# Performance work log

Hardware: AMD Instinct MI355X
Metric: run time of the kernel (lower is better)

## Reference

```python
import jax, jax.numpy as jnp
import numpy as np

N_S, N_T, E = 50000, 50000, 600000
D_IN, D_H, D_OUT = 256, 128, 64


def setup_inputs() -> dict:
    key = jax.random.key(0)
    k1, k2, k3, k4, k5, k6 = jax.random.split(key, 6)
    edge_src = jax.random.randint(k1, (E,), 0, N_S, dtype=jnp.int32)
    edge_dst = jax.random.randint(k2, (E,), 0, N_T, dtype=jnp.int32)
    edge_index = jnp.stack([edge_src, edge_dst], axis=0)  # [2, E]
    x_s = jax.random.normal(k3, (N_S, D_IN), dtype=jnp.float32)
    x_t = jax.random.normal(k4, (N_T, D_IN), dtype=jnp.float32)
    W0 = jax.random.normal(k5, (D_IN, D_H), dtype=jnp.float32) * (1.0 / np.sqrt(D_IN))
    W1 = jax.random.normal(k6, (D_H, D_OUT), dtype=jnp.float32) * (1.0 / np.sqrt(D_H))
    return {"edge_index": edge_index, "x_s": x_s, "x_t": x_t, "W0": W0, "W1": W1}


def gcn_conv(x, src, dst, W):
    """PyG GCNConv, bias=False: D^{-1/2}(A+I)D^{-1/2} (x @ W)."""
    N = x.shape[0]
    h = x @ W  # [N, out]
    loops = jnp.arange(N, dtype=src.dtype)
    s = jnp.concatenate([src, loops])  # add self-loops
    d = jnp.concatenate([dst, loops])
    deg = jax.ops.segment_sum(jnp.ones_like(d, dtype=h.dtype), d, num_segments=N)
    dinv = jnp.where(deg > 0, jax.lax.rsqrt(deg), 0.0)
    norm = dinv[s] * dinv[d]  # [E+N]
    return jax.ops.segment_sum(h[s] * norm[:, None], d, num_segments=N)


def reference(edge_index, x_s, x_t, W0, W1):
    n_s = x_s.shape[0]
    src = edge_index[0]
    dst = edge_index[1] + n_s  # targets live in the x_t block
    acts = [jax.nn.relu, lambda v: v]
    Ws = [W0, W1]
    for W, act in zip(Ws, acts):
        x = jnp.concatenate([x_s, x_t], axis=0)
        x = act(gcn_conv(x, src, dst, W))
        x_s, x_t = x[:n_s], x[n_s:]
    return (x_s, x_t)
```

## Files before the change

### kernel.cpp

```cpp
#include <hip/hip_runtime.h>
#include <cstdint>
#include <cstddef>

typedef unsigned short u16;
typedef unsigned int   u32;
typedef __attribute__((ext_vector_type(8))) short bf16x8;
typedef __attribute__((ext_vector_type(4))) float f32x4;

#define D_IN  256
#define D_H   128
#define D_OUT 64
#define LSTR  72

__device__ __forceinline__ float bf2f(u16 u){
  union { u32 i; float f; } v; v.i = ((u32)u) << 16; return v.f;
}
__device__ __forceinline__ u16 f2bf(float f){
  union { float f; u32 i; } v; v.f = f;
  u32 r = (v.i + 0x7fffu + ((v.i >> 16) & 1u)) >> 16;
  return (u16)r;
}

__global__ void k_wprep(const float* __restrict__ W0, const float* __restrict__ W1,
                        u16* __restrict__ W0t, u16* __restrict__ W1t,
                        int* __restrict__ deg, int n_t){
  int i = blockIdx.x * 256 + threadIdx.x;
  if (i < 128 * 256){
    int n = i >> 8, k = i & 255;
    W0t[i] = f2bf(W0[(size_t)k * 128 + n]);
  } else if (i < 128 * 256 + 64 * 128){
    int j = i - 128 * 256;
    int n = j >> 7, k = j & 127;
    W1t[j] = f2bf(W1[(size_t)k * 64 + n]);
  } else if (i - (128 * 256 + 64 * 128) < n_t){
    deg[i - (128 * 256 + 64 * 128)] = 0;
  }
}

__global__ void k_deg(const int* __restrict__ dst, int E, int* __restrict__ deg){
  int e = blockIdx.x * 256 + threadIdx.x;
  if (e < E) atomicAdd(&deg[dst[e]], 1);
}

__global__ __launch_bounds__(256) void k_bsum(const int* __restrict__ deg, int N,
                                              int* __restrict__ bsum){
  __shared__ int s[256];
  int tid = threadIdx.x;
  int i = blockIdx.x * 256 + tid;
  s[tid] = (i < N) ? deg[i] : 0;
  __syncthreads();
  for (int o = 128; o > 0; o >>= 1){
    if (tid < o) s[tid] += s[tid + o];
    __syncthreads();
  }
  if (tid == 0) bsum[blockIdx.x] = s[0];
}

__global__ __launch_bounds__(256) void k_off(const int* __restrict__ deg, int N,
                                             const int* __restrict__ bsum, int nb,
                                             int* __restrict__ off, int* __restrict__ cursor,
                                             float* __restrict__ dinv){
  __shared__ int s[256];
  __shared__ int sbase[256];
  const int tid = threadIdx.x;
  const int bid = blockIdx.x;
  const int i   = bid * 256 + tid;
  int acc = 0;
  for (int j = tid; j < bid; j += 256) acc += bsum[j];
  sbase[tid] = acc;
  int v = (i < N) ? deg[i] : 0;
  s[tid] = v;
  __syncthreads();
  for (int o = 128; o > 0; o >>= 1){
    if (tid < o) sbase[tid] += sbase[tid + o];
    __syncthreads();
  }
  for (int o = 1; o < 256; o <<= 1){
    int t = (tid >= o) ? s[tid - o] : 0;
    __syncthreads();
    s[tid] += t;
    __syncthreads();
  }
  if (i < N){
    int excl = s[tid] - v + sbase[0];
    off[i] = excl;
    cursor[i] = excl;
    dinv[i] = rsqrtf((float)v + 1.0f);
  }
}

__global__ void k_fill(const int* __restrict__ src, const int* __restrict__ dst,
                       int E, int* __restrict__ cursor, int* __restrict__ csr){
  int e = blockIdx.x * 256 + threadIdx.x;
  if (e < E){
    int d = dst[e];
    int p = atomicAdd(&cursor[d], 1);
    csr[p] = src[e];
  }
}

__global__ __launch_bounds__(256) void k_gemm1(
    const float* __restrict__ Xs, const float* __restrict__ Xt,
    const u16* __restrict__ W0t, int M, int n_s,
    u16* __restrict__ out)
{
  __shared__ u16 As[128 * LSTR];
  __shared__ u16 Bs[128 * LSTR];
  const int t    = threadIdx.x;
  const int wave = t >> 6, lane = t & 63;
  const int wm   = (wave >> 1) * 64, wn = (wave & 1) * 64;
  const int lm   = lane & 15, quad = lane >> 4;
  const int row0 = blockIdx.x * 128;

  f32x4 acc[4][4];
  const f32x4 z = {0.f, 0.f, 0.f, 0.f};
  #pragma unroll
  for (int i = 0; i < 4; i++)
    #pragma unroll
    for (int j = 0; j < 4; j++) acc[i][j] = z;

  const int ar = t >> 1;
  const int kh = (t & 1) * 32;
  const int r  = row0 + ar;
  const float* xp = nullptr;
  if (r < M) xp = (r < n_s) ? (Xs + (size_t)r * D_IN) : (Xt + (size_t)(r - n_s) * D_IN);
  const u16* wrow = W0t + (size_t)ar * D_IN + kh;

  float4 a4[8];
  int4   b4[4];
  if (xp){
    #pragma unroll
    for (int j = 0; j < 8; j++) a4[j] = *(const float4*)(xp + kh + j * 4);
  } else {
    float4 zz = make_float4(0,0,0,0);
    #pragma unroll
    for (int j = 0; j < 8; j++) a4[j] = zz;
  }
  #pragma unroll
  for (int j = 0; j < 4; j++) b4[j] = *(const int4*)(wrow + j * 8);

  for (int k0 = 0; k0 < D_IN; k0 += 64){
    __syncthreads();
    {
      u16 abuf[32];
      #pragma unroll
      for (int j = 0; j < 8; j++){
        abuf[j*4+0] = f2bf(a4[j].x); abuf[j*4+1] = f2bf(a4[j].y);
        abuf[j*4+2] = f2bf(a4[j].z); abuf[j*4+3] = f2bf(a4[j].w);
      }
      u16* ap = &As[ar * LSTR + kh];
      *(int4*)(ap +  0) = *(int4*)&abuf[0];
      *(int4*)(ap +  8) = *(int4*)&abuf[8];
      *(int4*)(ap + 16) = *(int4*)&abuf[16];
      *(int4*)(ap + 24) = *(int4*)&abuf[24];
      u16* bp = &Bs[ar * LSTR + kh];
      *(int4*)(bp +  0) = b4[0];
      *(int4*)(bp +  8) = b4[1];
      *(int4*)(bp + 16) = b4[2];
      *(int4*)(bp + 24) = b4[3];
    }
    __syncthreads();

    if (k0 + 64 < D_IN){
      if (xp){
        #pragma unroll
        for (int j = 0; j < 8; j++) a4[j] = *(const float4*)(xp + k0 + 64 + kh + j * 4);
      }
      #pragma unroll
      for (int j = 0; j < 4; j++) b4[j] = *(const int4*)(wrow + k0 + 64 + j * 8);
    }

    #pragma unroll
    for (int kk = 0; kk < 64; kk += 32){
      bf16x8 af[4], bfr[4];
      #pragma unroll
      for (int i = 0; i < 4; i++)
        af[i] = *(const bf16x8*)&As[(wm + i*16 + lm) * LSTR + kk + quad*8];
      #pragma unroll
      for (int i = 0; i < 4; i++)
        bfr[i] = *(const bf16x8*)&Bs[(wn + i*16 + lm) * LSTR + kk + quad*8];
      #pragma unroll
      for (int mi = 0; mi < 4; mi++)
        #pragma unroll
        for (int ni = 0; ni < 4; ni++)
          acc[mi][ni] = __builtin_amdgcn_mfma_f32_16x16x32_bf16(
              af[mi], bfr[ni], acc[mi][ni], 0, 0, 0);
    }
  }

  #pragma unroll
  for (int mi = 0; mi < 4; mi++){
    int rbase = row0 + wm + mi * 16 + quad * 4;
    #pragma unroll
    for (int rr = 0; rr < 4; rr++){
      int m = rbase + rr;
      if (m >= M) continue;
      u16* op = out + (size_t)m * D_H + wn + lm;
      #pragma unroll
      for (int ni = 0; ni < 4; ni++)
        op[ni * 16] = f2bf(acc[mi][ni][rr]);
    }
  }
}

__global__ __launch_bounds__(256) void k_aggf(
    const int* __restrict__ off, const int* __restrict__ deg,
    const int* __restrict__ csr, const float* __restrict__ dinv,
    u16* __restrict__ h1, int n_s, int n_t)
{
  int w    = (blockIdx.x * 256 + threadIdx.x) >> 6;
  int lane = threadIdx.x & 63;
  if (w >= n_t) return;
  const int g = lane >> 4;
  const int c = lane & 15;
  int start = off[w];
  int n     = deg[w];

  float r[8], p[8];
  #pragma unroll
  for (int q = 0; q < 8; q++){ r[q] = 0.f; p[q] = 0.f; }

  int i = 0;
  for (; i + 8 <= n; i += 8){
    int sa = csr[start + i + g];
    int sb = csr[start + i + 4 + g];
    int4 da = *(const int4*)(h1 + (size_t)sa * D_H + c * 8);
    int4 db = *(const int4*)(h1 + (size_t)sb * D_H + c * 8);
    const u16* ha = (const u16*)&da;
    const u16* hb = (const u16*)&db;
    #pragma unroll
    for (int q = 0; q < 8; q++){
      float va = bf2f(ha[q]), vb = bf2f(hb[q]);
      r[q] += va + vb;
      p[q] += fmaxf(va, 0.f) + fmaxf(vb, 0.f);
    }
  }
  for (; i < n; i += 4){
    if (i + g < n){
      int sa = csr[start + i + g];
      int4 da = *(const int4*)(h1 + (size_t)sa * D_H + c * 8);
      const u16* ha = (const u16*)&da;
      #pragma unroll
      for (int q = 0; q < 8; q++){
        float va = bf2f(ha[q]);
        r[q] += va;
        p[q] += fmaxf(va, 0.f);
      }
    }
  }

  #pragma unroll
  for (int q = 0; q < 8; q++){
    r[q] += __shfl_xor(r[q], 16, 64);
    r[q] += __shfl_xor(r[q], 32, 64);
    p[q] += __shfl_xor(p[q], 16, 64);
    p[q] += __shfl_xor(p[q], 32, 64);
  }

  if (g == 0){
    float di  = dinv[w];
    float di2 = di * di;
    u16* selfp = h1 + (size_t)(n_s + w) * D_H + c * 8;
    int4 hs = *(const int4*)selfp;
    const u16* hh = (const u16*)&hs;
    u16 ob[8];
    #pragma unroll
    for (int q = 0; q < 8; q++){
      float zq = fmaxf(di * r[q] + di2 * bf2f(hh[q]), 0.f);
      float uq = di * p[q] + di2 * zq;
      ob[q] = f2bf(uq);
    }
    *(int4*)selfp = *(int4*)ob;
  }
}

__global__ __launch_bounds__(256) void k_gemm2(
    const u16* __restrict__ h1, const u16* __restrict__ W1t,
    int M, int n_s, float* __restrict__ out)
{
  __shared__ u16 As[128 * LSTR];
  __shared__ u16 Bs[64 * LSTR];
  const int t    = threadIdx.x;
  const int wave = t >> 6, lane = t & 63;
  const int wm   = wave * 32;
  const int lm   = lane & 15, quad = lane >> 4;
  const int row0 = blockIdx.x * 128;

  f32x4 acc[2][4];
  const f32x4 z = {0.f, 0.f, 0.f, 0.f};
  #pragma unroll
  for (int i = 0; i < 2; i++)
    #pragma unroll
    for (int j = 0; j < 4; j++) acc[i][j] = z;

  const int ar = t >> 1;
  const int kh = (t & 1) * 32;
  const int r  = row0 + ar;
  const bool relu_a = (r < n_s);
  const int bn = t >> 2;
  const int bk = (t & 3) * 16;

  int4 a4[4], w4[2];
  if (r < M){
    const u16* hp = h1 + (size_t)r * D_H + kh;
    #pragma unroll
    for (int j = 0; j < 4; j++) a4[j] = *(const int4*)(hp + j * 8);
  } else {
    int4 zz = make_int4(0,0,0,0);
    #pragma unroll
    for (int j = 0; j < 4; j++) a4[j] = zz;
  }
  w4[0] = *(const int4*)(W1t + (size_t)bn * D_H + bk);
  w4[1] = *(const int4*)(W1t + (size_t)bn * D_H + bk + 8);

  for (int k0 = 0; k0 < D_H; k0 += 64){
    __syncthreads();
    {
      u16 abuf[32];
      #pragma unroll
      for (int j = 0; j < 4; j++){
        u16* hh = (u16*)&a4[j];
        #pragma unroll
        for (int q = 0; q < 8; q++){
          u16 v = hh[q];
          abuf[j*8+q] = (relu_a && (v & 0x8000u)) ? (u16)0 : v;
        }
      }
      u16* ap = &As[ar * LSTR + kh];
      *(int4*)(ap +  0) = *(int4*)&abuf[0];
      *(int4*)(ap +  8) = *(int4*)&abuf[8];
      *(int4*)(ap + 16) = *(int4*)&abuf[16];
      *(int4*)(ap + 24) = *(int4*)&abuf[24];
      u16* bp = &Bs[bn * LSTR + bk];
      *(int4*)(bp + 0) = w4[0];
      *(int4*)(bp + 8) = w4[1];
    }
    __syncthreads();

    if (k0 + 64 < D_H){
      if (r < M){
        const u16* hp = h1 + (size_t)r * D_H + k0 + 64 + kh;
        #pragma unroll
        for (int j = 0; j < 4; j++) a4[j] = *(const int4*)(hp + j * 8);
      }
      w4[0] = *(const int4*)(W1t + (size_t)bn * D_H + k0 + 64 + bk);
      w4[1] = *(const int4*)(W1t + (size_t)bn * D_H + k0 + 64 + bk + 8);
    }

    #pragma unroll
    for (int kk = 0; kk < 64; kk += 32){
      bf16x8 af[2], bfr[4];
      #pragma unroll
      for (int i = 0; i < 2; i++)
        af[i] = *(const bf16x8*)&As[(wm + i*16 + lm) * LSTR + kk + quad*8];
      #pragma unroll
      for (int i = 0; i < 4; i++)
        bfr[i] = *(const bf16x8*)&Bs[(i*16 + lm) * LSTR + kk + quad*8];
      #pragma unroll
      for (int mi = 0; mi < 2; mi++)
        #pragma unroll
        for (int ni = 0; ni < 4; ni++)
          acc[mi][ni] = __builtin_amdgcn_mfma_f32_16x16x32_bf16(
              af[mi], bfr[ni], acc[mi][ni], 0, 0, 0);
    }
  }

  #pragma unroll
  for (int mi = 0; mi < 2; mi++){
    int rbase = row0 + wm + mi * 16 + quad * 4;
    #pragma unroll
    for (int rr = 0; rr < 4; rr++){
      int m = rbase + rr;
      if (m >= M) continue;
      float* op = out + (size_t)m * D_OUT + lm;
      #pragma unroll
      for (int ni = 0; ni < 4; ni++)
        op[ni * 16] = acc[mi][ni][rr];
    }
  }
}

static inline size_t alup(size_t x){ return (x + 255) & ~(size_t)255; }

extern "C" void kernel_launch(void* const* d_in, const int* in_sizes, int n_in,
                              void* d_out, int out_size, void* d_ws, size_t ws_size,
                              hipStream_t stream)
{
  const int*   ei = (const int*)d_in[0];
  const float* xs = (const float*)d_in[1];
  const float* xt = (const float*)d_in[2];
  const float* W0 = (const float*)d_in[3];
  const float* W1 = (const float*)d_in[4];
  const int E   = in_sizes[0] / 2;
  const int n_s = in_sizes[1] / D_IN;
  const int n_t = in_sizes[2] / D_IN;
  const int M   = n_s + n_t;
  const int* src = ei;
  const int* dst = ei + E;
  const int nb_t = (n_t + 255) / 256;

  char* p = (char*)d_ws;
  int*   deg    = (int*)p;    p += alup((size_t)n_t * 4);
  int*   off    = (int*)p;    p += alup((size_t)n_t * 4);
  int*   cursor = (int*)p;    p += alup((size_t)n_t * 4);
  float* dinv   = (float*)p;  p += alup((size_t)n_t * 4);
  int*   bsum   = (int*)p;    p += alup((size_t)nb_t * 4);
  int*   csr    = (int*)p;    p += alup((size_t)E * 4);
  u16*   W0t    = (u16*)p;    p += alup((size_t)D_H * D_IN * 2);
  u16*   W1t    = (u16*)p;    p += alup((size_t)D_OUT * D_H * 2);
  u16*   h1     = (u16*)p;    p += alup((size_t)M * D_H * 2);

  const int wprep_n = 128*256 + 64*128 + n_t;
  k_wprep <<<(wprep_n + 255) / 256, 256, 0, stream>>>(W0, W1, W0t, W1t, deg, n_t);
  k_deg   <<<(E + 255) / 256, 256, 0, stream>>>(dst, E, deg);
  k_bsum  <<<nb_t, 256, 0, stream>>>(deg, n_t, bsum);
  k_off   <<<nb_t, 256, 0, stream>>>(deg, n_t, bsum, nb_t, off, cursor, dinv);
  k_fill  <<<(E + 255) / 256, 256, 0, stream>>>(src, dst, E, cursor, csr);

  k_gemm1<<<(M + 127) / 128, 256, 0, stream>>>(xs, xt, W0t, M, n_s, h1);
  k_aggf <<<(n_t + 3) / 4, 256, 0, stream>>>(off, deg, csr, dinv, h1, n_s, n_t);
  k_gemm2<<<(M + 127) / 128, 256, 0, stream>>>(h1, W1t, M, n_s, (float*)d_out);
}
```

Before: 279.2 us.

## Drop block-sum kernel, use packed bf16 conversion, single-stage gemm2 tile

Removes the k_bsum launch by having each k_off block sum all preceding degree entries directly, which saves a launch but makes later blocks read up to 50k ints each. In gemm1 the scalar float-to-bf16 rounding is replaced with the packed __float22bfloat162_rn intrinsic. gemm2 now loads the full K=128 slice into shared memory at once with a wider padded stride and runs all MFMAs after a single barrier, dropping the two-stage loop and its extra syncs.

```diff
diff --git a/kernel.cpp b/kernel.cpp
--- a/kernel.cpp
+++ b/kernel.cpp
@@ -1,4 +1,5 @@
 #include <hip/hip_runtime.h>
+#include <hip/hip_bf16.h>
 #include <cstdint>
 #include <cstddef>
 
@@ -11,6 +12,7 @@
 #define D_H   128
 #define D_OUT 64
 #define LSTR  72
+#define LSTR2 136
 
 __device__ __forceinline__ float bf2f(u16 u){
   union { u32 i; float f; } v; v.i = ((u32)u) << 16; return v.f;
@@ -42,22 +44,7 @@
   if (e < E) atomicAdd(&deg[dst[e]], 1);
 }
 
-__global__ __launch_bounds__(256) void k_bsum(const int* __restrict__ deg, int N,
-                                              int* __restrict__ bsum){
-  __shared__ int s[256];
-  int tid = threadIdx.x;
-  int i = blockIdx.x * 256 + tid;
-  s[tid] = (i < N) ? deg[i] : 0;
-  __syncthreads();
-  for (int o = 128; o > 0; o >>= 1){
-    if (tid < o) s[tid] += s[tid + o];
-    __syncthreads();
-  }
-  if (tid == 0) bsum[blockIdx.x] = s[0];
-}
-
 __global__ __launch_bounds__(256) void k_off(const int* __restrict__ deg, int N,
-                                             const int* __restrict__ bsum, int nb,
                                              int* __restrict__ off, int* __restrict__ cursor,
                                              float* __restrict__ dinv){
   __shared__ int s[256];
@@ -65,8 +52,9 @@
   const int tid = threadIdx.x;
   const int bid = blockIdx.x;
   const int i   = bid * 256 + tid;
+  const int lim = bid * 256;
   int acc = 0;
-  for (int j = tid; j < bid; j += 256) acc += bsum[j];
+  for (int j = tid; j < lim; j += 256) acc += deg[j];
   sbase[tid] = acc;
   int v = (i < N) ? deg[i] : 0;
   s[tid] = v;
@@ -142,17 +130,19 @@
   for (int k0 = 0; k0 < D_IN; k0 += 64){
     __syncthreads();
     {
-      u16 abuf[32];
+      union { int4 q[4]; u32 w[16]; } ab;
       #pragma unroll
       for (int j = 0; j < 8; j++){
-        abuf[j*4+0] = f2bf(a4[j].x); abuf[j*4+1] = f2bf(a4[j].y);
-        abuf[j*4+2] = f2bf(a4[j].z); abuf[j*4+3] = f2bf(a4[j].w);
+        __hip_bfloat162 p0 = __float22bfloat162_rn(float2{a4[j].x, a4[j].y});
+        __hip_bfloat162 p1 = __float22bfloat162_rn(float2{a4[j].z, a4[j].w});
+        ab.w[2*j]   = *(u32*)&p0;
+        ab.w[2*j+1] = *(u32*)&p1;
       }
       u16* ap = &As[ar * LSTR + kh];
-      *(int4*)(ap +  0) = *(int4*)&abuf[0];
-      *(int4*)(ap +  8) = *(int4*)&abuf[8];
-      *(int4*)(ap + 16) = *(int4*)&abuf[16];
-      *(int4*)(ap + 24) = *(int4*)&abuf[24];
+      *(int4*)(ap +  0) = ab.q[0];
+      *(int4*)(ap +  8) = ab.q[1];
+      *(int4*)(ap + 16) = ab.q[2];
+      *(int4*)(ap + 24) = ab.q[3];
       u16* bp = &Bs[ar * LSTR + kh];
       *(int4*)(bp +  0) = b4[0];
       *(int4*)(bp +  8) = b4[1];
@@ -278,91 +268,76 @@
     const u16* __restrict__ h1, const u16* __restrict__ W1t,
     int M, int n_s, float* __restrict__ out)
 {
-  __shared__ u16 As[128 * LSTR];
-  __shared__ u16 Bs[64 * LSTR];
+  __shared__ u16 As[128 * LSTR2];
+  __shared__ u16 Bs[64 * LSTR2];
   const int t    = threadIdx.x;
   const int wave = t >> 6, lane = t & 63;
   const int wm   = wave * 32;
   const int lm   = lane & 15, quad = lane >> 4;
   const int row0 = blockIdx.x * 128;
 
-  f32x4 acc[2][4];
-  const f32x4 z = {0.f, 0.f, 0.f, 0.f};
-  #pragma unroll
-  for (int i = 0; i < 2; i++)
-    #pragma unroll
-    for (int j = 0; j < 4; j++) acc[i][j] = z;
-
   const int ar = t >> 1;
-  const int kh = (t & 1) * 32;
+  const int kh = (t & 1) * 64;
   const int r  = row0 + ar;
   const bool relu_a = (r < n_s);
   const int bn = t >> 2;
-  const int bk = (t & 3) * 16;
-
-  int4 a4[4], w4[2];
-  if (r < M){
-    const u16* hp = h1 + (size_t)r * D_H + kh;
-    #pragma unroll
-    for (int j = 0; j < 4; j++) a4[j] = *(const int4*)(hp + j * 8);
-  } else {
-    int4 zz = make_int4(0,0,0,0);
-    #pragma unroll
-    for (int j = 0; j < 4; j++) a4[j] = zz;
-  }
-  w4[0] = *(const int4*)(W1t + (size_t)bn * D_H + bk);
-  w4[1] = *(const int4*)(W1t + (size_t)bn * D_H + bk + 8);
-
-  for (int k0 = 0; k0 < D_H; k0 += 64){
-    __syncthreads();
-    {
-      u16 abuf[32];
-      #pragma unroll
-      for (int j = 0; j < 4; j++){
-        u16* hh = (u16*)&a4[j];
+  const int bk = (t & 3) * 32;
+
+  {
+    int4 a4[8];
+    if (r < M){
+      const u16* hp = h1 + (size_t)r * D_H + kh;
+      #pragma unroll
+      for (int j = 0; j < 8; j++) a4[j] = *(const int4*)(hp + j * 8);
+    } else {
+      int4 zz = make_int4(0,0,0,0);
+      #pragma unroll
+      for (int j = 0; j < 8; j++) a4[j] = zz;
+    }
+    int4 w4[4];
+    const u16* wp = W1t + (size_t)bn * D_H + bk;
+    #pragma unroll
+    for (int j = 0; j < 4; j++) w4[j] = *(const int4*)(wp + j * 8);
+
+    u16* ap = &As[ar * LSTR2 + kh];
+    #pragma unroll
+    for (int j = 0; j < 8; j++){
+      u16* hh = (u16*)&a4[j];
+      if (relu_a){
         #pragma unroll
-        for (int q = 0; q < 8; q++){
-          u16 v = hh[q];
-          abuf[j*8+q] = (relu_a && (v & 0x8000u)) ? (u16)0 : v;
-        }
+        for (int q = 0; q < 8; q++)
+          hh[q] = (hh[q] & 0x8000u) ? (u16)0 : hh[q];
       }
-      u16* ap = &As[ar * LSTR + kh];
-      *(int4*)(ap +  0) = *(int4*)&abuf[0];
-      *(int4*)(ap +  8) = *(int4*)&abuf[8];
-      *(int4*)(ap + 16) = *(int4*)&abuf[16];
-      *(int4*)(ap + 24) = *(int4*)&abuf[24];
-      u16* bp = &Bs[bn * LSTR + bk];
-      *(int4*)(bp + 0) = w4[0];
-      *(int4*)(bp + 8) = w4[1];
-    }
-    __syncthreads();
-
-    if (k0 + 64 < D_H){
-      if (r < M){
-        const u16* hp = h1 + (size_t)r * D_H + k0 + 64 + kh;
-        #pragma unroll
-        for (int j = 0; j < 4; j++) a4[j] = *(const int4*)(hp + j * 8);
-      }
-      w4[0] = *(const int4*)(W1t + (size_t)bn * D_H + k0 + 64 + bk);
-      w4[1] = *(const int4*)(W1t + (size_t)bn * D_H + k0 + 64 + bk + 8);
-    }
-
-    #pragma unroll
-    for (int kk = 0; kk < 64; kk += 32){
-      bf16x8 af[2], bfr[4];
-      #pragma unroll
-      for (int i = 0; i < 2; i++)
-        af[i] = *(const bf16x8*)&As[(wm + i*16 + lm) * LSTR + kk + quad*8];
-      #pragma unroll
-      for (int i = 0; i < 4; i++)
-        bfr[i] = *(const bf16x8*)&Bs[(i*16 + lm) * LSTR + kk + quad*8];
-      #pragma unroll
-      for (int mi = 0; mi < 2; mi++)
-        #pragma unroll
-        for (int ni = 0; ni < 4; ni++)
-          acc[mi][ni] = __builtin_amdgcn_mfma_f32_16x16x32_bf16(
-              af[mi], bfr[ni], acc[mi][ni], 0, 0, 0);
-    }
+      *(int4*)(ap + j * 8) = a4[j];
+    }
+    u16* bp = &Bs[bn * LSTR2 + bk];
+    #pragma unroll
+    for (int j = 0; j < 4; j++) *(int4*)(bp + j * 8) = w4[j];
+  }
+  __syncthreads();
+
+  f32x4 acc[2][4];
+  const f32x4 z = {0.f, 0.f, 0.f, 0.f};
+  #pragma unroll
+  for (int i = 0; i < 2; i++)
+    #pragma unroll
+    for (int j = 0; j < 4; j++) acc[i][j] = z;
+
+  #pragma unroll
+  for (int kk = 0; kk < 128; kk += 32){
+    bf16x8 af[2], bfr[4];
+    #pragma unroll
+    for (int i = 0; i < 2; i++)
+      af[i] = *(const bf16x8*)&As[(wm + i*16 + lm) * LSTR2 + kk + quad*8];
+    #pragma unroll
+    for (int i = 0; i < 4; i++)
+      bfr[i] = *(const bf16x8*)&Bs[(i*16 + lm) * LSTR2 + kk + quad*8];
+    #pragma unroll
+    for (int mi = 0; mi < 2; mi++)
+      #pragma unroll
+      for (int ni = 0; ni < 4; ni++)
+        acc[mi][ni] = __builtin_amdgcn_mfma_f32_16x16x32_bf16(
+            af[mi], bfr[ni], acc[mi][ni], 0, 0, 0);
   }
 
   #pragma unroll
@@ -404,7 +379,6 @@
   int*   off    = (int*)p;    p += alup((size_t)n_t * 4);
   int*   cursor = (int*)p;    p += alup((size_t)n_t * 4);
   float* dinv   = (float*)p;  p += alup((size_t)n_t * 4);
-  int*   bsum   = (int*)p;    p += alup((size_t)nb_t * 4);
   int*   csr    = (int*)p;    p += alup((size_t)E * 4);
   u16*   W0t    = (u16*)p;    p += alup((size_t)D_H * D_IN * 2);
   u16*   W1t    = (u16*)p;    p += alup((size_t)D_OUT * D_H * 2);
@@ -413,8 +387,7 @@
   const int wprep_n = 128*256 + 64*128 + n_t;
   k_wprep <<<(wprep_n + 255) / 256, 256, 0, stream>>>(W0, W1, W0t, W1t, deg, n_t);
   k_deg   <<<(E + 255) / 256, 256, 0, stream>>>(dst, E, deg);
-  k_bsum  <<<nb_t, 256, 0, stream>>>(deg, n_t, bsum);
-  k_off   <<<nb_t, 256, 0, stream>>>(deg, n_t, bsum, nb_t, off, cursor, dinv);
+  k_off   <<<nb_t, 256, 0, stream>>>(deg, n_t, off, cursor, dinv);
   k_fill  <<<(E + 255) / 256, 256, 0, stream>>>(src, dst, E, cursor, csr);
 
   k_gemm1<<<(M + 127) / 128, 256, 0, stream>>>(xs, xt, W0t, M, n_s, h1);
```

New measurement: 298.3 us. 6.9% more time.
